# Optimization experiments

Measured on AMD Instinct MI355X. Metric: run time of the kernel, lower is better.

Reference implementation:

```python
import jax, jax.numpy as jnp
import numpy as np

NX = 96
N_NODES = 6 * NX * NX          # 55296 cubed-sphere grid points
N_EDGES = 4 * N_NODES          # ~4-neighbor connectivity
HID = 32
NUM_STEPS = 3


def setup_inputs() -> dict:
    key = jax.random.key(0)
    ks = jax.random.split(key, 12)
    s = 0.05
    inp = {
        "in_node_features": jax.random.normal(ks[0], (2, 6, NX, NX, 32), jnp.float32),
        "edge_relation": jax.random.normal(ks[1], (N_EDGES, 4), jnp.float32),
        "pw1": jax.random.normal(ks[2], (32, HID), jnp.float32) * s,
        "pb1": jnp.zeros((HID,), jnp.float32),
        "pw2": jax.random.normal(ks[3], (HID, HID), jnp.float32) * s,
        "pb2": jnp.zeros((HID,), jnp.float32),
        "ew1": jax.random.normal(ks[4], (4, 32), jnp.float32) * s,
        "eb1": jnp.zeros((32,), jnp.float32),
        "ew2": jax.random.normal(ks[5], (32, HID * HID), jnp.float32) * s,
        "eb2": jnp.zeros((HID * HID,), jnp.float32),
        "conv_b": jnp.zeros((HID,), jnp.float32),
        "gru_w_ih": jax.random.normal(ks[6], (3 * HID, HID), jnp.float32) * s,
        "gru_w_hh": jax.random.normal(ks[7], (3 * HID, HID), jnp.float32) * s,
        "gru_b_ih": jnp.zeros((3 * HID,), jnp.float32),
        "gru_b_hh": jnp.zeros((3 * HID,), jnp.float32),
        "edge_src": jax.random.randint(ks[8], (N_EDGES,), 0, N_NODES, jnp.int32),
        "edge_dst": jax.random.randint(ks[9], (N_EDGES,), 0, N_NODES, jnp.int32),
    }
    return inp


def reference(in_node_features, edge_relation, pw1, pb1, pw2, pb2,
              ew1, eb1, ew2, eb2, conv_b,
              gru_w_ih, gru_w_hh, gru_b_ih, gru_b_hh,
              edge_src, edge_dst):
    B, T, nx1, nx2, C = in_node_features.shape
    N = T * nx1 * nx2
    H = pw2.shape[1]

    x = in_node_features.reshape(B, N, C)
    # project_node_features: Linear -> ReLU -> Linear
    h0 = jnp.maximum(x @ pw1 + pb1, 0.0) @ pw2 + pb2          # [B, N, H]

    # edge network (same every step): Linear -> ReLU -> Linear -> [E, H, H]
    We = (jnp.maximum(edge_relation @ ew1 + eb1, 0.0) @ ew2 + eb2)
    We = We.reshape(-1, H, H)                                  # [E, H, H]

    def seg_sum(m):  # m: [E, H] -> [N, H]
        return jax.ops.segment_sum(m, edge_dst, num_segments=N)

    def step(carry, _):
        node, hidden = carry                                   # each [B, N, H]
        # NNConv: gather src feats, per-edge matmul, scatter-sum to dst
        msg = jnp.einsum('beh,eho->beo', node[:, edge_src], We)  # [B, E, H]
        agg = jax.vmap(seg_sum)(msg) + conv_b                    # [B, N, H]
        node = jnp.maximum(agg, 0.0)                             # ReLU
        # single GRU step (seq_len = 1)
        gx = node @ gru_w_ih.T + gru_b_ih                        # [B, N, 3H]
        gh = hidden @ gru_w_hh.T + gru_b_hh
        r = jax.nn.sigmoid(gx[..., :H] + gh[..., :H])
        z = jax.nn.sigmoid(gx[..., H:2 * H] + gh[..., H:2 * H])
        n = jnp.tanh(gx[..., 2 * H:] + r * gh[..., 2 * H:])
        hidden = (1.0 - z) * n + z * hidden
        return (hidden, hidden), None

    (node, _), _ = jax.lax.scan(step, (h0, h0), None, length=NUM_STEPS)
    return node.reshape(B, T, nx1, nx2, H)
```

## Files before the change

kernel.cpp:

```cpp
#include <hip/hip_runtime.h>

typedef unsigned short u16;
typedef short s16x8 __attribute__((ext_vector_type(8)));
typedef float f32x4 __attribute__((ext_vector_type(4)));
typedef float f32x2 __attribute__((ext_vector_type(2)));

#define NNODES 55296
#define NEDGES 221184
#define ROWS   110592
#define NBLK_SCAN 216

__device__ __forceinline__ u16 f2bf(float f) {
    union { float f; unsigned u; } v; v.f = f;
    unsigned r = (v.u + 0x7fffu + ((v.u >> 16) & 1u)) >> 16;
    return (u16)r;
}
__device__ __forceinline__ float bf2f(u16 u) {
    return __uint_as_float(((unsigned)u) << 16);
}

__global__ __launch_bounds__(256) void hist_kernel(
    const int* __restrict__ edst, int* __restrict__ cnt)
{
    int i = blockIdx.x * 256 + threadIdx.x;
    atomicAdd(&cnt[edst[i]], 1);
}

__global__ __launch_bounds__(256) void scan1_kernel(
    const int* __restrict__ cnt, int* __restrict__ exc, int* __restrict__ bsum)
{
    __shared__ int s[256];
    int t = threadIdx.x, g = blockIdx.x * 256 + t;
    int v = cnt[g];
    s[t] = v; __syncthreads();
#pragma unroll
    for (int d = 1; d < 256; d <<= 1) {
        int x = (t >= d) ? s[t - d] : 0;
        __syncthreads();
        s[t] += x;
        __syncthreads();
    }
    exc[g] = s[t] - v;
    if (t == 255) bsum[blockIdx.x] = s[255];
}

__global__ __launch_bounds__(256) void scan2_kernel(
    const int* __restrict__ bsum, int* __restrict__ bofs)
{
    __shared__ int s[256];
    int t = threadIdx.x;
    int v = (t < NBLK_SCAN) ? bsum[t] : 0;
    s[t] = v; __syncthreads();
#pragma unroll
    for (int d = 1; d < 256; d <<= 1) {
        int x = (t >= d) ? s[t - d] : 0;
        __syncthreads();
        s[t] += x;
        __syncthreads();
    }
    if (t < NBLK_SCAN) bofs[t] = s[t] - v;
}

__global__ __launch_bounds__(256) void scatter_kernel(
    const int* __restrict__ edst, const int* __restrict__ esrc,
    const int* __restrict__ exc, const int* __restrict__ bofs,
    int* __restrict__ cnt,
    int* __restrict__ perm, int* __restrict__ esrcp, int* __restrict__ edstp)
{
    int i = blockIdx.x * 256 + threadIdx.x;
    int d = edst[i];
    int slot = atomicSub(&cnt[d], 1) - 1;
    int pos = exc[d] + bofs[d >> 8] + slot;
    perm[pos] = i;
    esrcp[pos] = esrc[i];
    edstp[pos] = d;
}

__global__ __launch_bounds__(256) void pack_all(
    const float* __restrict__ ew2, u16* __restrict__ ew2f,
    const float* __restrict__ pw1, u16* __restrict__ pw1h, u16* __restrict__ pw1l,
    const float* __restrict__ pw2, u16* __restrict__ pw2h, u16* __restrict__ pw2l,
    const float* __restrict__ wih, u16* __restrict__ wihh, u16* __restrict__ wihl,
    const float* __restrict__ whh, u16* __restrict__ whhh, u16* __restrict__ whhl)
{
    int b = blockIdx.x;
    const float* src; u16 *hi, *lo; int ncols, trans, base;
    if (b < 128)      { src = ew2; hi = ew2f; lo = nullptr; ncols = 1024; trans = 0; base = 0;   }
    else if (b < 132) { src = pw1; hi = pw1h; lo = pw1l;    ncols = 32;   trans = 0; base = 128; }
    else if (b < 136) { src = pw2; hi = pw2h; lo = pw2l;    ncols = 32;   trans = 0; base = 132; }
    else if (b < 148) { src = wih; hi = wihh; lo = wihl;    ncols = 96;   trans = 1; base = 136; }
    else              { src = whh; hi = whhh; lo = whhl;    ncols = 96;   trans = 1; base = 148; }
    int idx = (b - base) * 256 + threadIdx.x;
    int t = idx >> 9, rr = idx & 511, lane = rr >> 3, j = rr & 7;
    int k = (lane >> 4) * 8 + j;
    int n = t * 16 + (lane & 15);
    float v = trans ? src[n * 32 + k] : src[k * ncols + n];
    u16 hb = f2bf(v);
    hi[idx] = hb;
    if (lo) lo[idx] = f2bf(v - bf2f(hb));
}

__global__ __launch_bounds__(256) void edgemlp_kernel(
    const float* __restrict__ er, const float* __restrict__ ew1,
    const float* __restrict__ eb1, const int* __restrict__ perm,
    u16* __restrict__ rbf)
{
    __shared__ float er_lds[32];
    __shared__ float w_lds[128];
    __shared__ float b_lds[32];
    int tid = threadIdx.x;
    int e8 = blockIdx.x * 8;
    if (tid < 32) {
        int e = perm[e8 + (tid >> 2)];
        er_lds[tid] = er[e * 4 + (tid & 3)];
    }
    else if (tid < 160) w_lds[tid - 32] = ew1[tid - 32];
    else if (tid < 192) b_lds[tid - 160] = eb1[tid - 160];
    __syncthreads();
    int el = tid >> 5, o = tid & 31;
    const float* e4 = er_lds + el * 4;
    float v = b_lds[o] + e4[0] * w_lds[o] + e4[1] * w_lds[32 + o]
                       + e4[2] * w_lds[64 + o] + e4[3] * w_lds[96 + o];
    rbf[(e8 + el) * 32 + o] = f2bf(fmaxf(v, 0.f));
}

__global__ __launch_bounds__(256) void nodeproj_kernel(
    const float* __restrict__ x,
    const u16* __restrict__ pw1h, const u16* __restrict__ pw1l, const float* __restrict__ pb1,
    const u16* __restrict__ pw2h, const u16* __restrict__ pw2l, const float* __restrict__ pb2,
    float* __restrict__ st_f32, u16* __restrict__ st_hi, u16* __restrict__ st_lo)
{
    __shared__ alignas(16) u16 t_hi[4][512];
    __shared__ alignas(16) u16 t_lo[4][512];
    int tid = threadIdx.x, wave = tid >> 6, lane = tid & 63;
    int quad = lane >> 4, col = lane & 15;
    int row0 = (blockIdx.x * 4 + wave) * 16;

    const float* xp = x + (row0 + col) * 32 + quad * 8;
    f32x4 xv0 = *(const f32x4*)(xp), xv1 = *(const f32x4*)(xp + 4);
    s16x8 ah, al;
#pragma unroll
    for (int i = 0; i < 4; ++i) {
        u16 h0 = f2bf(xv0[i]); ah[i] = (short)h0; al[i] = (short)f2bf(xv0[i] - bf2f(h0));
        u16 h1 = f2bf(xv1[i]); ah[4+i] = (short)h1; al[4+i] = (short)f2bf(xv1[i] - bf2f(h1));
    }
#pragma unroll
    for (int t = 0; t < 2; ++t) {
        s16x8 bh = *(const s16x8*)(pw1h + t * 512 + lane * 8);
        s16x8 bl = *(const s16x8*)(pw1l + t * 512 + lane * 8);
        f32x4 acc = {0,0,0,0};
        acc = __builtin_amdgcn_mfma_f32_16x16x32_bf16(al, bh, acc, 0,0,0);
        acc = __builtin_amdgcn_mfma_f32_16x16x32_bf16(ah, bl, acc, 0,0,0);
        acc = __builtin_amdgcn_mfma_f32_16x16x32_bf16(ah, bh, acc, 0,0,0);
        float bias = pb1[t * 16 + col];
#pragma unroll
        for (int r = 0; r < 4; ++r) {
            float v = fmaxf(acc[r] + bias, 0.f);
            u16 hb = f2bf(v);
            int idx = (quad * 4 + r) * 32 + t * 16 + col;
            t_hi[wave][idx] = hb;
            t_lo[wave][idx] = f2bf(v - bf2f(hb));
        }
    }
    __syncthreads();
    s16x8 th = *(const s16x8*)(&t_hi[wave][col * 32 + quad * 8]);
    s16x8 tl = *(const s16x8*)(&t_lo[wave][col * 32 + quad * 8]);
#pragma unroll
    for (int t = 0; t < 2; ++t) {
        s16x8 bh = *(const s16x8*)(pw2h + t * 512 + lane * 8);
        s16x8 bl = *(const s16x8*)(pw2l + t * 512 + lane * 8);
        f32x4 acc = {0,0,0,0};
        acc = __builtin_amdgcn_mfma_f32_16x16x32_bf16(tl, bh, acc, 0,0,0);
        acc = __builtin_amdgcn_mfma_f32_16x16x32_bf16(th, bl, acc, 0,0,0);
        acc = __builtin_amdgcn_mfma_f32_16x16x32_bf16(th, bh, acc, 0,0,0);
        float bias = pb2[t * 16 + col];
#pragma unroll
        for (int r = 0; r < 4; ++r) {
            float v = acc[r] + bias;
            int row = row0 + quad * 4 + r;
            int o = t * 16 + col;
            st_f32[row * 32 + o] = v;
            u16 hb = f2bf(v);
            st_hi[row * 32 + o] = hb;
            st_lo[row * 32 + o] = f2bf(v - bf2f(hb));
        }
    }
}

__global__ __launch_bounds__(256) void msg_kernel(
    const u16* __restrict__ rbf, const u16* __restrict__ ew2f,
    const float* __restrict__ eb2, const float* __restrict__ state,
    const int* __restrict__ esrcp, const int* __restrict__ edstp,
    float* __restrict__ agg)
{
    __shared__ alignas(16) float eb2_lds[1024];
    __shared__ alignas(16) float ns_lds[4][32 * 68];
    int tid = threadIdx.x;
    {
        *(f32x4*)(eb2_lds + tid * 4) = *(const f32x4*)(eb2 + tid * 4);
    }
    int wave = tid >> 6, lane = tid & 63;
    int quad = lane >> 4, col = lane & 15;
    int e0 = (blockIdx.x * 4 + wave) * 32;

    s16x8 afrag0 = *(const s16x8*)(rbf + (size_t)(e0 + col) * 32 + quad * 8);
    s16x8 afrag1 = *(const s16x8*)(rbf + (size_t)(e0 + 16 + col) * 32 + quad * 8);

#pragma unroll
    for (int i = 0; i < 2; ++i) {
        int t2 = i * 64 + lane;
        int el = t2 >> 2, hc = t2 & 3;
        int src = esrcp[e0 + el];
        const float* s0 = state + (size_t)src * 32 + hc * 8;
        const float* s1 = state + ((size_t)NNODES + src) * 32 + hc * 8;
        f32x4 a0 = *(const f32x4*)(s0),     a1 = *(const f32x4*)(s0 + 4);
        f32x4 c0 = *(const f32x4*)(s1),     c1 = *(const f32x4*)(s1 + 4);
        float* dp = &ns_lds[wave][el * 68 + hc * 16];
        f32x4 w0 = {a0.x, c0.x, a0.y, c0.y};
        f32x4 w1 = {a0.z, c0.z, a0.w, c0.w};
        f32x4 w2 = {a1.x, c1.x, a1.y, c1.y};
        f32x4 w3 = {a1.z, c1.z, a1.w, c1.w};
        *(f32x4*)(dp + 0)  = w0;
        *(f32x4*)(dp + 4)  = w1;
        *(f32x4*)(dp + 8)  = w2;
        *(f32x4*)(dp + 12) = w3;
    }
    int dstid[8];
#pragma unroll
    for (int g = 0; g < 2; ++g)
#pragma unroll
        for (int r = 0; r < 4; ++r)
            dstid[g * 4 + r] = edstp[e0 + g * 16 + quad * 4 + r];
    __syncthreads();

    f32x2 m[2][2][4];
#pragma unroll
    for (int g = 0; g < 2; ++g)
#pragma unroll
        for (int oh = 0; oh < 2; ++oh)
#pragma unroll
            for (int r = 0; r < 4; ++r) m[g][oh][r] = f32x2{0.f, 0.f};

    const float* nsw = &ns_lds[wave][0];
#pragma unroll 2
    for (int hh = 0; hh < 16; ++hh) {
        int h0 = hh * 2, h1 = hh * 2 + 1;
        s16x8 b0 = *(const s16x8*)(ew2f + (4 * hh + 0) * 512 + lane * 8);
        s16x8 b1 = *(const s16x8*)(ew2f + (4 * hh + 1) * 512 + lane * 8);
        s16x8 b2 = *(const s16x8*)(ew2f + (4 * hh + 2) * 512 + lane * 8);
        s16x8 b3 = *(const s16x8*)(ew2f + (4 * hh + 3) * 512 + lane * 8);
        f32x4 z = {0,0,0,0};
        f32x4 d[2][4];
        d[0][0] = __builtin_amdgcn_mfma_f32_16x16x32_bf16(afrag0, b0, z, 0,0,0);
        d[0][1] = __builtin_amdgcn_mfma_f32_16x16x32_bf16(afrag0, b1, z, 0,0,0);
        d[0][2] = __builtin_amdgcn_mfma_f32_16x16x32_bf16(afrag0, b2, z, 0,0,0);
        d[0][3] = __builtin_amdgcn_mfma_f32_16x16x32_bf16(afrag0, b3, z, 0,0,0);
        d[1][0] = __builtin_amdgcn_mfma_f32_16x16x32_bf16(afrag1, b0, z, 0,0,0);
        d[1][1] = __builtin_amdgcn_mfma_f32_16x16x32_bf16(afrag1, b1, z, 0,0,0);
        d[1][2] = __builtin_amdgcn_mfma_f32_16x16x32_bf16(afrag1, b2, z, 0,0,0);
        d[1][3] = __builtin_amdgcn_mfma_f32_16x16x32_bf16(afrag1, b3, z, 0,0,0);
        float e00 = eb2_lds[h0 * 32 + col],  e01 = eb2_lds[h0 * 32 + 16 + col];
        float e10 = eb2_lds[h1 * 32 + col],  e11 = eb2_lds[h1 * 32 + 16 + col];
#pragma unroll
        for (int g = 0; g < 2; ++g) {
#pragma unroll
            for (int r = 0; r < 4; ++r) {
                int e = g * 16 + quad * 4 + r;
                f32x4 nv = *(const f32x4*)(nsw + e * 68 + hh * 4);
                f32x2 nh0 = {nv.x, nv.y};
                f32x2 nh1 = {nv.z, nv.w};
                float w00 = d[g][0][r] + e00, w01 = d[g][1][r] + e01;
                float w10 = d[g][2][r] + e10, w11 = d[g][3][r] + e11;
                m[g][0][r] += nh0 * w00 + nh1 * w10;
                m[g][1][r] += nh0 * w01 + nh1 * w11;
            }
        }
    }
#pragma unroll
    for (int g = 0; g < 2; ++g) {
        bool valid[4] = {true, true, true, true};
#pragma unroll
        for (int r = 3; r >= 1; --r) {
            if (dstid[g * 4 + r] == dstid[g * 4 + r - 1]) {
                valid[r] = false;
                m[g][0][r-1] += m[g][0][r];
                m[g][1][r-1] += m[g][1][r];
            }
        }
#pragma unroll
        for (int r = 0; r < 4; ++r) {
            if (valid[r]) {
                float* p0 = agg + (size_t)dstid[g * 4 + r] * 32;
                float* p1 = agg + ((size_t)NNODES + dstid[g * 4 + r]) * 32;
                unsafeAtomicAdd(p0 + col,      m[g][0][r].x);
                unsafeAtomicAdd(p0 + 16 + col, m[g][1][r].x);
                unsafeAtomicAdd(p1 + col,      m[g][0][r].y);
                unsafeAtomicAdd(p1 + 16 + col, m[g][1][r].y);
            }
        }
    }
}

__global__ __launch_bounds__(256) void gru_kernel(
    const float* __restrict__ agg, const float* __restrict__ conv_b,
    const float* __restrict__ st_f32, const u16* __restrict__ st_hi, const u16* __restrict__ st_lo,
    const u16* __restrict__ wihh, const u16* __restrict__ wihl,
    const u16* __restrict__ whhh, const u16* __restrict__ whhl,
    const float* __restrict__ b_ih, const float* __restrict__ b_hh,
    float* __restrict__ out_f32, u16* __restrict__ out_hi, u16* __restrict__ out_lo)
{
    int tid = threadIdx.x, wave = tid >> 6, lane = tid & 63;
    int quad = lane >> 4, col = lane & 15;
    int row0 = (blockIdx.x * 4 + wave) * 16;

    const float* ap = agg + (row0 + col) * 32 + quad * 8;
    f32x4 av0 = *(const f32x4*)(ap), av1 = *(const f32x4*)(ap + 4);
    const float* cb = conv_b + quad * 8;
    f32x4 cb0 = *(const f32x4*)(cb), cb1 = *(const f32x4*)(cb + 4);
    s16x8 anh, anl;
#pragma unroll
    for (int i = 0; i < 4; ++i) {
        float v0 = fmaxf(av0[i] + cb0[i], 0.f);
        float v1 = fmaxf(av1[i] + cb1[i], 0.f);
        u16 h0 = f2bf(v0); anh[i] = (short)h0;   anl[i] = (short)f2bf(v0 - bf2f(h0));
        u16 h1 = f2bf(v1); anh[4+i] = (short)h1; anl[4+i] = (short)f2bf(v1 - bf2f(h1));
    }
    s16x8 ahh = *(const s16x8*)(st_hi + (row0 + col) * 32 + quad * 8);
    s16x8 ahl = *(const s16x8*)(st_lo + (row0 + col) * 32 + quad * 8);

    f32x4 gx[6], gh[6];
#pragma unroll
    for (int t = 0; t < 6; ++t) {
        s16x8 bh = *(const s16x8*)(wihh + t * 512 + lane * 8);
        s16x8 bl = *(const s16x8*)(wihl + t * 512 + lane * 8);
        f32x4 acc = {0,0,0,0};
        acc = __builtin_amdgcn_mfma_f32_16x16x32_bf16(anl, bh, acc, 0,0,0);
        acc = __builtin_amdgcn_mfma_f32_16x16x32_bf16(anh, bl, acc, 0,0,0);
        acc = __builtin_amdgcn_mfma_f32_16x16x32_bf16(anh, bh, acc, 0,0,0);
        gx[t] = acc;
        s16x8 ch = *(const s16x8*)(whhh + t * 512 + lane * 8);
        s16x8 cl = *(const s16x8*)(whhl + t * 512 + lane * 8);
        f32x4 acc2 = {0,0,0,0};
        acc2 = __builtin_amdgcn_mfma_f32_16x16x32_bf16(ahl, ch, acc2, 0,0,0);
        acc2 = __builtin_amdgcn_mfma_f32_16x16x32_bf16(ahh, cl, acc2, 0,0,0);
        acc2 = __builtin_amdgcn_mfma_f32_16x16x32_bf16(ahh, ch, acc2, 0,0,0);
        gh[t] = acc2;
    }
    float bihv[6], bhhv[6];
#pragma unroll
    for (int t = 0; t < 6; ++t) { bihv[t] = b_ih[t * 16 + col]; bhhv[t] = b_hh[t * 16 + col]; }

#pragma unroll
    for (int r = 0; r < 4; ++r) {
        int row = row0 + quad * 4 + r;
#pragma unroll
        for (int oh = 0; oh < 2; ++oh) {
            int o = oh * 16 + col;
            float hid = st_f32[row * 32 + o];
            float sr = (gx[oh][r] + bihv[oh]) + (gh[oh][r] + bhhv[oh]);
            float sz = (gx[2+oh][r] + bihv[2+oh]) + (gh[2+oh][r] + bhhv[2+oh]);
            float gxn = gx[4+oh][r] + bihv[4+oh];
            float ghn = gh[4+oh][r] + bhhv[4+oh];
            float rr = 1.f / (1.f + __expf(-sr));
            float zz = 1.f / (1.f + __expf(-sz));
            float narg = gxn + rr * ghn;
            float ex = __expf(2.f * narg);
            float nn = (ex - 1.f) / (ex + 1.f);
            float hnew = (1.f - zz) * nn + zz * hid;
            out_f32[row * 32 + o] = hnew;
            u16 hb = f2bf(hnew);
            out_hi[row * 32 + o] = hb;
            out_lo[row * 32 + o] = f2bf(hnew - bf2f(hb));
        }
    }
}

extern "C" void kernel_launch(void* const* d_in, const int* in_sizes, int n_in,
                              void* d_out, int out_size, void* d_ws, size_t ws_size,
                              hipStream_t stream)
{
    const float* x      = (const float*)d_in[0];
    const float* er     = (const float*)d_in[1];
    const float* pw1    = (const float*)d_in[2];
    const float* pb1    = (const float*)d_in[3];
    const float* pw2    = (const float*)d_in[4];
    const float* pb2    = (const float*)d_in[5];
    const float* ew1    = (const float*)d_in[6];
    const float* eb1    = (const float*)d_in[7];
    const float* ew2    = (const float*)d_in[8];
    const float* eb2    = (const float*)d_in[9];
    const float* conv_b = (const float*)d_in[10];
    const float* wih    = (const float*)d_in[11];
    const float* whh    = (const float*)d_in[12];
    const float* bih    = (const float*)d_in[13];
    const float* bhh    = (const float*)d_in[14];
    const int*   esrc   = (const int*)d_in[15];
    const int*   edst   = (const int*)d_in[16];
    float* out = (float*)d_out;

    char* ws = (char*)d_ws;
    size_t off = 0;
    auto alloc = [&](size_t bytes) -> void* {
        void* p = ws + off;
        off = (off + bytes + 255) & ~(size_t)255;
        return p;
    };
    u16*   rbf    = (u16*)  alloc((size_t)(NEDGES + 32) * 32 * 2);
    float* st_f32 = (float*)alloc((size_t)ROWS * 32 * 4);
    u16*   st_hi  = (u16*)  alloc((size_t)ROWS * 32 * 2);
    u16*   st_lo  = (u16*)  alloc((size_t)ROWS * 32 * 2);
    float* agg    = (float*)alloc((size_t)ROWS * 32 * 4);
    u16*   ew2f   = (u16*)  alloc(64 * 512 * 2);
    u16*   pw1h   = (u16*)  alloc(2 * 512 * 2);
    u16*   pw1l   = (u16*)  alloc(2 * 512 * 2);
    u16*   pw2h   = (u16*)  alloc(2 * 512 * 2);
    u16*   pw2l   = (u16*)  alloc(2 * 512 * 2);
    u16*   wihhf  = (u16*)  alloc(6 * 512 * 2);
    u16*   wihlf  = (u16*)  alloc(6 * 512 * 2);
    u16*   whhhf  = (u16*)  alloc(6 * 512 * 2);
    u16*   whhlf  = (u16*)  alloc(6 * 512 * 2);
    int*   cnt      = (int*)alloc((size_t)NNODES * 4);
    int*   exc      = (int*)alloc((size_t)NNODES * 4);
    int*   bsum     = (int*)alloc(NBLK_SCAN * 4);
    int*   bofs     = (int*)alloc(NBLK_SCAN * 4);
    int*   perm     = (int*)alloc((size_t)NEDGES * 4);
    int*   esrcp    = (int*)alloc((size_t)(NEDGES + 32) * 4);
    int*   edstp    = (int*)alloc((size_t)(NEDGES + 32) * 4);
    (void)in_sizes; (void)n_in; (void)out_size; (void)ws_size;

    hipMemsetAsync(cnt, 0, (size_t)NNODES * 4, stream);
    hist_kernel<<<NEDGES / 256, 256, 0, stream>>>(edst, cnt);
    scan1_kernel<<<NBLK_SCAN, 256, 0, stream>>>(cnt, exc, bsum);
    scan2_kernel<<<1, 256, 0, stream>>>(bsum, bofs);
    scatter_kernel<<<NEDGES / 256, 256, 0, stream>>>(edst, esrc, exc, bofs, cnt,
                                                     perm, esrcp, edstp);

    pack_all<<<160, 256, 0, stream>>>(ew2, ew2f, pw1, pw1h, pw1l, pw2, pw2h, pw2l,
                                      wih, wihhf, wihlf, whh, whhhf, whhlf);

    edgemlp_kernel<<<NEDGES / 8, 256, 0, stream>>>(er, ew1, eb1, perm, rbf);
    nodeproj_kernel<<<ROWS / 64, 256, 0, stream>>>(x, pw1h, pw1l, pb1, pw2h, pw2l, pb2,
                                                   st_f32, st_hi, st_lo);
    for (int s = 0; s < 3; ++s) {
        hipMemsetAsync(agg, 0, (size_t)ROWS * 32 * 4, stream);
        msg_kernel<<<NEDGES / 128, 256, 0, stream>>>(rbf, ew2f, eb2, st_f32,
                                                     esrcp, edstp, agg);
        float* of = (s == 2) ? out : st_f32;
        gru_kernel<<<ROWS / 64, 256, 0, stream>>>(agg, conv_b, st_f32, st_hi, st_lo,
                                                  wihhf, wihlf, whhhf, whhlf, bih, bhh,
                                                  of, st_hi, st_lo);
    }
}
```

Measured before the change: 379.4 us.

## Fold agg zeroing into kernels, halve edges per wave in msg, batch edge MLP

Result: no change. 385.6 us (+1.6%).

```diff
diff --git a/kernel.cpp b/kernel.cpp
--- a/kernel.cpp
+++ b/kernel.cpp
@@ -105,30 +105,37 @@
     const float* __restrict__ eb1, const int* __restrict__ perm,
     u16* __restrict__ rbf)
 {
-    __shared__ float er_lds[32];
+    __shared__ float er_lds[128];
     __shared__ float w_lds[128];
     __shared__ float b_lds[32];
     int tid = threadIdx.x;
-    int e8 = blockIdx.x * 8;
-    if (tid < 32) {
-        int e = perm[e8 + (tid >> 2)];
+    int e32 = blockIdx.x * 32;
+    if (tid < 128) {
+        int e = perm[e32 + (tid >> 2)];
         er_lds[tid] = er[e * 4 + (tid & 3)];
-    }
-    else if (tid < 160) w_lds[tid - 32] = ew1[tid - 32];
-    else if (tid < 192) b_lds[tid - 160] = eb1[tid - 160];
+    } else {
+        w_lds[tid - 128] = ew1[tid - 128];
+    }
+    if (tid < 32) b_lds[tid] = eb1[tid];
     __syncthreads();
-    int el = tid >> 5, o = tid & 31;
-    const float* e4 = er_lds + el * 4;
-    float v = b_lds[o] + e4[0] * w_lds[o] + e4[1] * w_lds[32 + o]
-                       + e4[2] * w_lds[64 + o] + e4[3] * w_lds[96 + o];
-    rbf[(e8 + el) * 32 + o] = f2bf(fmaxf(v, 0.f));
+    int el0 = tid >> 5, o = tid & 31;
+    float bo = b_lds[o];
+    float w0 = w_lds[o], w1 = w_lds[32 + o], w2 = w_lds[64 + o], w3 = w_lds[96 + o];
+#pragma unroll
+    for (int i = 0; i < 4; ++i) {
+        int el = el0 + i * 8;
+        const float* e4 = er_lds + el * 4;
+        float v = bo + e4[0] * w0 + e4[1] * w1 + e4[2] * w2 + e4[3] * w3;
+        rbf[(e32 + el) * 32 + o] = f2bf(fmaxf(v, 0.f));
+    }
 }
 
 __global__ __launch_bounds__(256) void nodeproj_kernel(
     const float* __restrict__ x,
     const u16* __restrict__ pw1h, const u16* __restrict__ pw1l, const float* __restrict__ pb1,
     const u16* __restrict__ pw2h, const u16* __restrict__ pw2l, const float* __restrict__ pb2,
-    float* __restrict__ st_f32, u16* __restrict__ st_hi, u16* __restrict__ st_lo)
+    float* __restrict__ st_f32, u16* __restrict__ st_hi, u16* __restrict__ st_lo,
+    float* __restrict__ agg)
 {
     __shared__ alignas(16) u16 t_hi[4][512];
     __shared__ alignas(16) u16 t_lo[4][512];
@@ -136,7 +143,13 @@
     int quad = lane >> 4, col = lane & 15;
     int row0 = (blockIdx.x * 4 + wave) * 16;
 
-    const float* xp = x + (row0 + col) * 32 + quad * 8;
+    {
+        f32x4 z = {0,0,0,0};
+        float* zp = agg + (size_t)(row0 + col) * 32 + quad * 8;
+        *(f32x4*)(zp) = z; *(f32x4*)(zp + 4) = z;
+    }
+
+    const float* xp = x + (size_t)(row0 + col) * 32 + quad * 8;
     f32x4 xv0 = *(const f32x4*)(xp), xv1 = *(const f32x4*)(xp + 4);
     s16x8 ah, al;
 #pragma unroll
@@ -179,10 +192,10 @@
             float v = acc[r] + bias;
             int row = row0 + quad * 4 + r;
             int o = t * 16 + col;
-            st_f32[row * 32 + o] = v;
+            st_f32[(size_t)row * 32 + o] = v;
             u16 hb = f2bf(v);
-            st_hi[row * 32 + o] = hb;
-            st_lo[row * 32 + o] = f2bf(v - bf2f(hb));
+            st_hi[(size_t)row * 32 + o] = hb;
+            st_lo[(size_t)row * 32 + o] = f2bf(v - bf2f(hb));
         }
     }
 }
@@ -194,27 +207,24 @@
     float* __restrict__ agg)
 {
     __shared__ alignas(16) float eb2_lds[1024];
-    __shared__ alignas(16) float ns_lds[4][32 * 68];
+    __shared__ alignas(16) float ns_lds[4][16 * 68];
     int tid = threadIdx.x;
     {
         *(f32x4*)(eb2_lds + tid * 4) = *(const f32x4*)(eb2 + tid * 4);
     }
     int wave = tid >> 6, lane = tid & 63;
     int quad = lane >> 4, col = lane & 15;
-    int e0 = (blockIdx.x * 4 + wave) * 32;
-
-    s16x8 afrag0 = *(const s16x8*)(rbf + (size_t)(e0 + col) * 32 + quad * 8);
-    s16x8 afrag1 = *(const s16x8*)(rbf + (size_t)(e0 + 16 + col) * 32 + quad * 8);
-
-#pragma unroll
-    for (int i = 0; i < 2; ++i) {
-        int t2 = i * 64 + lane;
-        int el = t2 >> 2, hc = t2 & 3;
+    int e0 = (blockIdx.x * 4 + wave) * 16;
+
+    s16x8 afrag = *(const s16x8*)(rbf + (size_t)(e0 + col) * 32 + quad * 8);
+
+    {
+        int el = lane >> 2, hc = lane & 3;
         int src = esrcp[e0 + el];
         const float* s0 = state + (size_t)src * 32 + hc * 8;
         const float* s1 = state + ((size_t)NNODES + src) * 32 + hc * 8;
-        f32x4 a0 = *(const f32x4*)(s0),     a1 = *(const f32x4*)(s0 + 4);
-        f32x4 c0 = *(const f32x4*)(s1),     c1 = *(const f32x4*)(s1 + 4);
+        f32x4 a0 = *(const f32x4*)(s0), a1 = *(const f32x4*)(s0 + 4);
+        f32x4 c0 = *(const f32x4*)(s1), c1 = *(const f32x4*)(s1 + 4);
         float* dp = &ns_lds[wave][el * 68 + hc * 16];
         f32x4 w0 = {a0.x, c0.x, a0.y, c0.y};
         f32x4 w1 = {a0.z, c0.z, a0.w, c0.w};
@@ -225,24 +235,19 @@
         *(f32x4*)(dp + 8)  = w2;
         *(f32x4*)(dp + 12) = w3;
     }
-    int dstid[8];
-#pragma unroll
-    for (int g = 0; g < 2; ++g)
-#pragma unroll
-        for (int r = 0; r < 4; ++r)
-            dstid[g * 4 + r] = edstp[e0 + g * 16 + quad * 4 + r];
+    int dstid[4];
+#pragma unroll
+    for (int r = 0; r < 4; ++r) dstid[r] = edstp[e0 + quad * 4 + r];
     __syncthreads();
 
-    f32x2 m[2][2][4];
-#pragma unroll
-    for (int g = 0; g < 2; ++g)
-#pragma unroll
-        for (int oh = 0; oh < 2; ++oh)
-#pragma unroll
-            for (int r = 0; r < 4; ++r) m[g][oh][r] = f32x2{0.f, 0.f};
+    f32x2 m[2][4];
+#pragma unroll
+    for (int oh = 0; oh < 2; ++oh)
+#pragma unroll
+        for (int r = 0; r < 4; ++r) m[oh][r] = f32x2{0.f, 0.f};
 
     const float* nsw = &ns_lds[wave][0];
-#pragma unroll 2
+#pragma unroll 4
     for (int hh = 0; hh < 16; ++hh) {
         int h0 = hh * 2, h1 = hh * 2 + 1;
         s16x8 b0 = *(const s16x8*)(ew2f + (4 * hh + 0) * 512 + lane * 8);
@@ -250,59 +255,48 @@
         s16x8 b2 = *(const s16x8*)(ew2f + (4 * hh + 2) * 512 + lane * 8);
         s16x8 b3 = *(const s16x8*)(ew2f + (4 * hh + 3) * 512 + lane * 8);
         f32x4 z = {0,0,0,0};
-        f32x4 d[2][4];
-        d[0][0] = __builtin_amdgcn_mfma_f32_16x16x32_bf16(afrag0, b0, z, 0,0,0);
-        d[0][1] = __builtin_amdgcn_mfma_f32_16x16x32_bf16(afrag0, b1, z, 0,0,0);
-        d[0][2] = __builtin_amdgcn_mfma_f32_16x16x32_bf16(afrag0, b2, z, 0,0,0);
-        d[0][3] = __builtin_amdgcn_mfma_f32_16x16x32_bf16(afrag0, b3, z, 0,0,0);
-        d[1][0] = __builtin_amdgcn_mfma_f32_16x16x32_bf16(afrag1, b0, z, 0,0,0);
-        d[1][1] = __builtin_amdgcn_mfma_f32_16x16x32_bf16(afrag1, b1, z, 0,0,0);
-        d[1][2] = __builtin_amdgcn_mfma_f32_16x16x32_bf16(afrag1, b2, z, 0,0,0);
-        d[1][3] = __builtin_amdgcn_mfma_f32_16x16x32_bf16(afrag1, b3, z, 0,0,0);
+        f32x4 d0 = __builtin_amdgcn_mfma_f32_16x16x32_bf16(afrag, b0, z, 0,0,0);
+        f32x4 d1 = __builtin_amdgcn_mfma_f32_16x16x32_bf16(afrag, b1, z, 0,0,0);
+        f32x4 d2 = __builtin_amdgcn_mfma_f32_16x16x32_bf16(afrag, b2, z, 0,0,0);
+        f32x4 d3 = __builtin_amdgcn_mfma_f32_16x16x32_bf16(afrag, b3, z, 0,0,0);
         float e00 = eb2_lds[h0 * 32 + col],  e01 = eb2_lds[h0 * 32 + 16 + col];
         float e10 = eb2_lds[h1 * 32 + col],  e11 = eb2_lds[h1 * 32 + 16 + col];
 #pragma unroll
-        for (int g = 0; g < 2; ++g) {
-#pragma unroll
-            for (int r = 0; r < 4; ++r) {
-                int e = g * 16 + quad * 4 + r;
-                f32x4 nv = *(const f32x4*)(nsw + e * 68 + hh * 4);
-                f32x2 nh0 = {nv.x, nv.y};
-                f32x2 nh1 = {nv.z, nv.w};
-                float w00 = d[g][0][r] + e00, w01 = d[g][1][r] + e01;
-                float w10 = d[g][2][r] + e10, w11 = d[g][3][r] + e11;
-                m[g][0][r] += nh0 * w00 + nh1 * w10;
-                m[g][1][r] += nh0 * w01 + nh1 * w11;
-            }
-        }
-    }
-#pragma unroll
-    for (int g = 0; g < 2; ++g) {
-        bool valid[4] = {true, true, true, true};
-#pragma unroll
-        for (int r = 3; r >= 1; --r) {
-            if (dstid[g * 4 + r] == dstid[g * 4 + r - 1]) {
-                valid[r] = false;
-                m[g][0][r-1] += m[g][0][r];
-                m[g][1][r-1] += m[g][1][r];
-            }
-        }
-#pragma unroll
         for (int r = 0; r < 4; ++r) {
-            if (valid[r]) {
-                float* p0 = agg + (size_t)dstid[g * 4 + r] * 32;
-                float* p1 = agg + ((size_t)NNODES + dstid[g * 4 + r]) * 32;
-                unsafeAtomicAdd(p0 + col,      m[g][0][r].x);
-                unsafeAtomicAdd(p0 + 16 + col, m[g][1][r].x);
-                unsafeAtomicAdd(p1 + col,      m[g][0][r].y);
-                unsafeAtomicAdd(p1 + 16 + col, m[g][1][r].y);
-            }
+            int e = quad * 4 + r;
+            f32x4 nv = *(const f32x4*)(nsw + e * 68 + hh * 4);
+            f32x2 nh0 = {nv.x, nv.y};
+            f32x2 nh1 = {nv.z, nv.w};
+            float w00 = d0[r] + e00, w01 = d1[r] + e01;
+            float w10 = d2[r] + e10, w11 = d3[r] + e11;
+            m[0][r] += nh0 * w00 + nh1 * w10;
+            m[1][r] += nh0 * w01 + nh1 * w11;
+        }
+    }
+    bool valid[4] = {true, true, true, true};
+#pragma unroll
+    for (int r = 3; r >= 1; --r) {
+        if (dstid[r] == dstid[r - 1]) {
+            valid[r] = false;
+            m[0][r-1] += m[0][r];
+            m[1][r-1] += m[1][r];
+        }
+    }
+#pragma unroll
+    for (int r = 0; r < 4; ++r) {
+        if (valid[r]) {
+            float* p0 = agg + (size_t)dstid[r] * 32;
+            float* p1 = agg + ((size_t)NNODES + dstid[r]) * 32;
+            unsafeAtomicAdd(p0 + col,      m[0][r].x);
+            unsafeAtomicAdd(p0 + 16 + col, m[1][r].x);
+            unsafeAtomicAdd(p1 + col,      m[0][r].y);
+            unsafeAtomicAdd(p1 + 16 + col, m[1][r].y);
         }
     }
 }
 
 __global__ __launch_bounds__(256) void gru_kernel(
-    const float* __restrict__ agg, const float* __restrict__ conv_b,
+    float* __restrict__ agg, const float* __restrict__ conv_b,
     const float* __restrict__ st_f32, const u16* __restrict__ st_hi, const u16* __restrict__ st_lo,
     const u16* __restrict__ wihh, const u16* __restrict__ wihl,
     const u16* __restrict__ whhh, const u16* __restrict__ whhl,
@@ -313,8 +307,12 @@
     int quad = lane >> 4, col = lane & 15;
     int row0 = (blockIdx.x * 4 + wave) * 16;
 
-    const float* ap = agg + (row0 + col) * 32 + quad * 8;
+    float* ap = agg + (size_t)(row0 + col) * 32 + quad * 8;
     f32x4 av0 = *(const f32x4*)(ap), av1 = *(const f32x4*)(ap + 4);
+    {
+        f32x4 z = {0,0,0,0};
+        *(f32x4*)(ap) = z; *(f32x4*)(ap + 4) = z;
+    }
     const float* cb = conv_b + quad * 8;
     f32x4 cb0 = *(const f32x4*)(cb), cb1 = *(const f32x4*)(cb + 4);
     s16x8 anh, anl;
@@ -325,8 +323,8 @@
         u16 h0 = f2bf(v0); anh[i] = (short)h0;   anl[i] = (short)f2bf(v0 - bf2f(h0));
         u16 h1 = f2bf(v1); anh[4+i] = (short)h1; anl[4+i] = (short)f2bf(v1 - bf2f(h1));
     }
-    s16x8 ahh = *(const s16x8*)(st_hi + (row0 + col) * 32 + quad * 8);
-    s16x8 ahl = *(const s16x8*)(st_lo + (row0 + col) * 32 + quad * 8);
+    s16x8 ahh = *(const s16x8*)(st_hi + (size_t)(row0 + col) * 32 + quad * 8);
+    s16x8 ahl = *(const s16x8*)(st_lo + (size_t)(row0 + col) * 32 + quad * 8);
 
     f32x4 gx[6], gh[6];
 #pragma unroll
@@ -356,7 +354,7 @@
 #pragma unroll
         for (int oh = 0; oh < 2; ++oh) {
             int o = oh * 16 + col;
-            float hid = st_f32[row * 32 + o];
+            float hid = st_f32[(size_t)row * 32 + o];
             float sr = (gx[oh][r] + bihv[oh]) + (gh[oh][r] + bhhv[oh]);
             float sz = (gx[2+oh][r] + bihv[2+oh]) + (gh[2+oh][r] + bhhv[2+oh]);
             float gxn = gx[4+oh][r] + bihv[4+oh];
@@ -367,10 +365,10 @@
             float ex = __expf(2.f * narg);
             float nn = (ex - 1.f) / (ex + 1.f);
             float hnew = (1.f - zz) * nn + zz * hid;
-            out_f32[row * 32 + o] = hnew;
+            out_f32[(size_t)row * 32 + o] = hnew;
             u16 hb = f2bf(hnew);
-            out_hi[row * 32 + o] = hb;
-            out_lo[row * 32 + o] = f2bf(hnew - bf2f(hb));
+            out_hi[(size_t)row * 32 + o] = hb;
+            out_lo[(size_t)row * 32 + o] = f2bf(hnew - bf2f(hb));
         }
     }
 }
@@ -438,13 +436,12 @@
     pack_all<<<160, 256, 0, stream>>>(ew2, ew2f, pw1, pw1h, pw1l, pw2, pw2h, pw2l,
                                       wih, wihhf, wihlf, whh, whhhf, whhlf);
 
-    edgemlp_kernel<<<NEDGES / 8, 256, 0, stream>>>(er, ew1, eb1, perm, rbf);
+    edgemlp_kernel<<<NEDGES / 32, 256, 0, stream>>>(er, ew1, eb1, perm, rbf);
     nodeproj_kernel<<<ROWS / 64, 256, 0, stream>>>(x, pw1h, pw1l, pb1, pw2h, pw2l, pb2,
-                                                   st_f32, st_hi, st_lo);
+                                                   st_f32, st_hi, st_lo, agg);
     for (int s = 0; s < 3; ++s) {
-        hipMemsetAsync(agg, 0, (size_t)ROWS * 32 * 4, stream);
-        msg_kernel<<<NEDGES / 128, 256, 0, stream>>>(rbf, ew2f, eb2, st_f32,
-                                                     esrcp, edstp, agg);
+        msg_kernel<<<NEDGES / 64, 256, 0, stream>>>(rbf, ew2f, eb2, st_f32,
+                                                    esrcp, edstp, agg);
         float* of = (s == 2) ? out : st_f32;
         gru_kernel<<<ROWS / 64, 256, 0, stream>>>(agg, conv_b, st_f32, st_hi, st_lo,
                                                   wihhf, wihlf, whhhf, whhlf, bih, bhh,
```
